# Kernel tuning notes

Hardware: AMD Instinct MI355X
Metric: run time of the kernel (lower is better)

Reference implementation:

```python
import jax, jax.numpy as jnp
import numpy as np

N_NODES = 80000
N_EDGES = 1280000
IN_C, HID_C, OUT_C = 128, 64, 40


def setup_inputs() -> dict:
    key = jax.random.key(0)
    k1, k2, k3, k4 = jax.random.split(key, 4)
    x = jax.random.normal(k1, (N_NODES, IN_C), dtype=jnp.float32)
    edge_index = jax.random.randint(k2, (2, N_EDGES), 0, N_NODES, dtype=jnp.int32)
    W1 = jax.random.normal(k3, (IN_C, HID_C), dtype=jnp.float32) * (1.0 / np.sqrt(IN_C))
    W2 = jax.random.normal(k4, (HID_C, OUT_C), dtype=jnp.float32) * (1.0 / np.sqrt(HID_C))
    return {"x": x, "edge_index": edge_index, "W1": W1, "W2": W2}


def _spmm_add(edge_index, h):
    # adj_t.matmul(h): out[dst] += h[src]  (aggr='add', message = x_j)
    src, dst = edge_index[0], edge_index[1]
    return jax.ops.segment_sum(h[src], dst, num_segments=N_NODES)


def reference(x, edge_index, W1, W2):
    # GCNConv 1: linear (no bias) then add-aggregate SpMM
    h = _spmm_add(edge_index, x @ W1)          # [N, HID]
    h = jax.nn.relu(h)
    # GCNConv 2
    h = _spmm_add(edge_index, h @ W2)          # [N, OUT]
    return jax.nn.log_softmax(h, axis=-1)
```

## Files before the change

kernel.cpp:

```cpp
#include <hip/hip_runtime.h>
#include <hip/hip_bf16.h>
#include <math.h>

#define N_NODES 80000
#define N_EDGES 1280000
#define IN_C 128
#define HID_C 64
#define OUT_C 40

#define KB 157
#define BK_CAP 10240
#define EPT 16

__device__ __forceinline__ float bf_lo(unsigned u) {
    union { unsigned i; float f; } c; c.i = u << 16; return c.f;
}
__device__ __forceinline__ float bf_hi(unsigned u) {
    union { unsigned i; float f; } c; c.i = u & 0xffff0000u; return c.f;
}
__device__ __forceinline__ unsigned pack_bf2(float a, float b) {
    union { float f; unsigned i; } ca, cb; ca.f = a; cb.f = b;
    unsigned ra = (ca.i + 0x7fffu + ((ca.i >> 16) & 1u)) >> 16;
    unsigned rb = (cb.i + 0x7fffu + ((cb.i >> 16) & 1u)) >> 16;
    return ra | (rb << 16);
}

typedef short v8s __attribute__((ext_vector_type(8)));
typedef float v4f __attribute__((ext_vector_type(4)));
union U16 { uint4 u; v8s s; };

__global__ void prep_w_kernel(const float* __restrict__ W1, const float* __restrict__ W2,
                              unsigned* __restrict__ w1t, unsigned* __restrict__ w2t,
                              int* __restrict__ bcnt) {
    const int tid = threadIdx.x;
    if (tid < KB) bcnt[tid] = 0;
    for (int i = tid; i < 4096; i += 256) {
        const int wcol = i >> 6, kk = i & 63;
        w1t[i] = pack_bf2(W1[(2 * kk) * HID_C + wcol], W1[(2 * kk + 1) * HID_C + wcol]);
    }
    for (int i = tid; i < 1536; i += 256) {
        const int wcol = i >> 5, kk = i & 31;
        w2t[i] = (wcol < OUT_C)
            ? pack_bf2(W2[(2 * kk) * OUT_C + wcol], W2[(2 * kk + 1) * OUT_C + wcol])
            : 0u;
    }
}

__global__ void binA_kernel(const int* __restrict__ src, const int* __restrict__ dst,
                            int* __restrict__ bcnt, int* __restrict__ gbuf) {
    __shared__ int lcnt[KB];
    __shared__ int lexcl[KB];
    __shared__ int lbase[KB];
    __shared__ int lcur[KB];
    __shared__ int stage[256 * EPT];
    __shared__ int gaddr[256 * EPT];
    const int tid = threadIdx.x;

    for (int i = tid; i < KB; i += 256) lcnt[i] = 0;
    __syncthreads();

    const int e0 = blockIdx.x * 256 * EPT;
    int my_s[EPT], my_b[EPT], my_dl[EPT];
#pragma unroll
    for (int j = 0; j < EPT; ++j) {
        const int e = e0 + j * 256 + tid;
        if (e < N_EDGES) {
            const int d = dst[e];
            my_s[j] = src[e];
            my_b[j] = d >> 9;
            my_dl[j] = d & 511;
            atomicAdd(&lcnt[my_b[j]], 1);
        } else my_b[j] = -1;
    }
    __syncthreads();

    if (tid < KB) lexcl[tid] = lcnt[tid];
    __syncthreads();
    for (int o = 1; o < KB; o <<= 1) {
        int t = (tid < KB && tid >= o) ? lexcl[tid - o] : 0;
        __syncthreads();
        if (tid < KB) lexcl[tid] += t;
        __syncthreads();
    }
    const int total = lexcl[KB - 1];
    if (tid < KB) {
        lexcl[tid] -= lcnt[tid];
        lbase[tid] = (lcnt[tid] > 0) ? atomicAdd(&bcnt[tid], lcnt[tid]) : 0;
        lcur[tid] = 0;
    }
    __syncthreads();

#pragma unroll
    for (int j = 0; j < EPT; ++j) {
        if (my_b[j] >= 0) {
            const int b = my_b[j];
            const int r = atomicAdd(&lcur[b], 1);
            const int li = lexcl[b] + r;
            stage[li] = (my_s[j] << 9) | my_dl[j];
            int gp = lbase[b] + r;
            if (gp >= BK_CAP) gp = BK_CAP - 1;
            gaddr[li] = b * BK_CAP + gp;
        }
    }
    __syncthreads();

    for (int i = tid; i < total; i += 256)
        gbuf[gaddr[i]] = stage[i];
}

__global__ void binB_kernel(const int* __restrict__ bcnt,
                            const int* __restrict__ gbuf,
                            int* __restrict__ rp, int* __restrict__ col) {
    __shared__ int sc[KB];
    __shared__ int hist[512];
    __shared__ int excl[512];
    __shared__ int cur[512];
    __shared__ int ps[256];
    __shared__ int outb[BK_CAP];
    const int b = blockIdx.x;
    const int tid = threadIdx.x;

    if (tid < KB) sc[tid] = min(bcnt[tid], BK_CAP);
    __syncthreads();
    for (int o = 1; o < KB; o <<= 1) {
        int t = (tid < KB && tid >= o) ? sc[tid - o] : 0;
        __syncthreads();
        if (tid < KB) sc[tid] += t;
        __syncthreads();
    }
    const int n = min(bcnt[b], BK_CAP);
    const int cbase = sc[b] - n;
    const int* __restrict__ my = gbuf + (size_t)b * BK_CAP;

    for (int i = tid; i < 512; i += 256) hist[i] = 0;
    __syncthreads();
    for (int i = tid; i < n; i += 256)
        atomicAdd(&hist[my[i] & 511], 1);
    __syncthreads();

    const int h0 = hist[2 * tid], h1 = hist[2 * tid + 1];
    const int p = h0 + h1;
    ps[tid] = p;
    __syncthreads();
    for (int o = 1; o < 256; o <<= 1) {
        int t = (tid >= o) ? ps[tid - o] : 0;
        __syncthreads();
        ps[tid] += t;
        __syncthreads();
    }
    const int pb = ps[tid] - p;
    excl[2 * tid] = pb;
    excl[2 * tid + 1] = pb + h0;
    cur[2 * tid] = pb;
    cur[2 * tid + 1] = pb + h0;
    __syncthreads();

    for (int i = tid; i < 512; i += 256) {
        const int node = b * 512 + i;
        if (node <= N_NODES) rp[node] = cbase + excl[i];
    }

    for (int i = tid; i < n; i += 256) {
        const int pk = my[i];
        const int pos = atomicAdd(&cur[pk & 511], 1);
        outb[pos] = pk >> 9;
    }
    __syncthreads();
    for (int i = tid; i < n; i += 256)
        col[cbase + i] = outb[i];
}

__global__ __launch_bounds__(256) void gemm1_kernel(const float* __restrict__ x,
                                                    const unsigned* __restrict__ w1t,
                                                    unsigned* __restrict__ h1b) {
    const int wave = threadIdx.x >> 6, lane = threadIdx.x & 63;
    const int nl = lane & 15, quad = lane >> 4;
    const int node = (blockIdx.x * 4 + wave) * 16 + nl;

    v4f acc[4];
#pragma unroll
    for (int q = 0; q < 4; ++q) acc[q] = (v4f){0.f, 0.f, 0.f, 0.f};

#pragma unroll
    for (int kit = 0; kit < 4; ++kit) {
        const float* xp = x + (size_t)node * IN_C + kit * 32 + quad * 8;
        const float4 lo = *(const float4*)xp;
        const float4 hi = *(const float4*)(xp + 4);
        U16 bu;
        bu.u.x = pack_bf2(lo.x, lo.y); bu.u.y = pack_bf2(lo.z, lo.w);
        bu.u.z = pack_bf2(hi.x, hi.y); bu.u.w = pack_bf2(hi.z, hi.w);
#pragma unroll
        for (int mt = 0; mt < 4; ++mt) {
            U16 au;
            au.u = *(const uint4*)(w1t + ((mt * 16 + nl) * 64 + kit * 16 + quad * 4));
            acc[mt] = __builtin_amdgcn_mfma_f32_16x16x32_bf16(au.s, bu.s, acc[mt], 0, 0, 0);
        }
    }
#pragma unroll
    for (int mt = 0; mt < 4; ++mt) {
        uint2 o;
        o.x = pack_bf2(acc[mt][0], acc[mt][1]);
        o.y = pack_bf2(acc[mt][2], acc[mt][3]);
        *(uint2*)(h1b + (size_t)node * 32 + mt * 8 + quad * 2) = o;
    }
}

__global__ void gather64_kernel(const int* __restrict__ rp, const int* __restrict__ col,
                                const unsigned* __restrict__ h1b,
                                unsigned* __restrict__ agg1b) {
    const int lane = threadIdx.x & 63;
    const int wave = threadIdx.x >> 6;
    const int sl = lane & 31;
    const int es = sl >> 3;
    const int cl = sl & 7;
    const int gbase = lane & 32;
    const int node = blockIdx.x * 8 + wave * 2 + (lane >> 5);
    const int b = rp[node], e = rp[node + 1];

    float acc[8];
#pragma unroll
    for (int k = 0; k < 8; ++k) acc[k] = 0.f;

    for (int pos = b; __any(pos < e); pos += 32) {
        const int rem = e - pos;
        const int n = rem > 32 ? 32 : (rem > 0 ? rem : 0);
        const int myIdx = (sl < n) ? col[pos + sl] : 0;
        const int steps = (n + 3) >> 2;
        int j = 0;
        for (; j + 1 < steps; j += 2) {
            const int e0 = (j << 2) + es, e1 = e0 + 4;
            const int s0 = __shfl(myIdx, gbase + e0, 64);
            const int s1 = __shfl(myIdx, gbase + e1, 64);
            uint4 v0, v1;
            const bool g0 = e0 < n, g1 = e1 < n;
            if (g0) v0 = *(const uint4*)(h1b + (size_t)s0 * 32 + cl * 4);
            if (g1) v1 = *(const uint4*)(h1b + (size_t)s1 * 32 + cl * 4);
            if (g0) {
                acc[0] += bf_lo(v0.x); acc[1] += bf_hi(v0.x);
                acc[2] += bf_lo(v0.y); acc[3] += bf_hi(v0.y);
                acc[4] += bf_lo(v0.z); acc[5] += bf_hi(v0.z);
                acc[6] += bf_lo(v0.w); acc[7] += bf_hi(v0.w);
            }
            if (g1) {
                acc[0] += bf_lo(v1.x); acc[1] += bf_hi(v1.x);
                acc[2] += bf_lo(v1.y); acc[3] += bf_hi(v1.y);
                acc[4] += bf_lo(v1.z); acc[5] += bf_hi(v1.z);
                acc[6] += bf_lo(v1.w); acc[7] += bf_hi(v1.w);
            }
        }
        if (j < steps) {
            const int e0 = (j << 2) + es;
            const int s0 = __shfl(myIdx, gbase + e0, 64);
            if (e0 < n) {
                const uint4 v = *(const uint4*)(h1b + (size_t)s0 * 32 + cl * 4);
                acc[0] += bf_lo(v.x); acc[1] += bf_hi(v.x);
                acc[2] += bf_lo(v.y); acc[3] += bf_hi(v.y);
                acc[4] += bf_lo(v.z); acc[5] += bf_hi(v.z);
                acc[6] += bf_lo(v.w); acc[7] += bf_hi(v.w);
            }
        }
    }
#pragma unroll
    for (int k = 0; k < 8; ++k) acc[k] += __shfl_down(acc[k], 16, 64);
#pragma unroll
    for (int k = 0; k < 8; ++k) acc[k] += __shfl_down(acc[k], 8, 64);

    if (sl < 8) {
        uint4 o;
        o.x = pack_bf2(fmaxf(acc[0], 0.f), fmaxf(acc[1], 0.f));
        o.y = pack_bf2(fmaxf(acc[2], 0.f), fmaxf(acc[3], 0.f));
        o.z = pack_bf2(fmaxf(acc[4], 0.f), fmaxf(acc[5], 0.f));
        o.w = pack_bf2(fmaxf(acc[6], 0.f), fmaxf(acc[7], 0.f));
        *(uint4*)(agg1b + (size_t)node * 32 + cl * 4) = o;
    }
}

__global__ __launch_bounds__(256) void gemm2_kernel(const unsigned* __restrict__ agg1b,
                                                    const unsigned* __restrict__ w2t,
                                                    unsigned* __restrict__ h2b) {
    const int wave = threadIdx.x >> 6, lane = threadIdx.x & 63;
    const int nl = lane & 15, quad = lane >> 4;
    const int node = (blockIdx.x * 4 + wave) * 16 + nl;

    v4f acc[3];
#pragma unroll
    for (int q = 0; q < 3; ++q) acc[q] = (v4f){0.f, 0.f, 0.f, 0.f};

#pragma unroll
    for (int kit = 0; kit < 2; ++kit) {
        U16 bu;
        bu.u = *(const uint4*)(agg1b + (size_t)node * 32 + kit * 16 + quad * 4);
#pragma unroll
        for (int mt = 0; mt < 3; ++mt) {
            U16 au;
            au.u = *(const uint4*)(w2t + ((mt * 16 + nl) * 32 + kit * 16 + quad * 4));
            acc[mt] = __builtin_amdgcn_mfma_f32_16x16x32_bf16(au.s, bu.s, acc[mt], 0, 0, 0);
        }
    }
#pragma unroll
    for (int mt = 0; mt < 2; ++mt) {
        uint2 o;
        o.x = pack_bf2(acc[mt][0], acc[mt][1]);
        o.y = pack_bf2(acc[mt][2], acc[mt][3]);
        *(uint2*)(h2b + (size_t)node * 20 + mt * 8 + quad * 2) = o;
    }
    if (quad < 2) {
        uint2 o;
        o.x = pack_bf2(acc[2][0], acc[2][1]);
        o.y = pack_bf2(acc[2][2], acc[2][3]);
        *(uint2*)(h2b + (size_t)node * 20 + 16 + quad * 2) = o;
    }
}

__global__ void gather40_ls_kernel(const int* __restrict__ rp, const int* __restrict__ col,
                                   const unsigned* __restrict__ h2b,
                                   float* __restrict__ out) {
    const int lane = threadIdx.x & 63;
    const int wave = threadIdx.x >> 6;
    const int sl = lane & 15;
    const int es = sl / 5;
    const int cl = sl - es * 5;
    const int gbase = lane & 48;
    const int node = blockIdx.x * 16 + wave * 4 + (lane >> 4);
    const int b = rp[node], e = rp[node + 1];

    float a[8];
#pragma unroll
    for (int k = 0; k < 8; ++k) a[k] = 0.f;

    for (int pos = b; __any(pos < e); pos += 16) {
        const int rem = e - pos;
        const int n = rem > 16 ? 16 : (rem > 0 ? rem : 0);
        const int myIdx = (sl < n) ? col[pos + sl] : 0;
        const int steps = (n + 2) / 3;
        int j = 0;
        for (; j + 1 < steps; j += 2) {
            const int e0 = j * 3 + es, e1 = e0 + 3;
            const int s0 = __shfl(myIdx, gbase + e0, 64);
            const int s1 = __shfl(myIdx, gbase + e1, 64);
            uint4 v0, v1;
            const bool g0 = (es < 3) && (e0 < n), g1 = (es < 3) && (e1 < n);
            if (g0) v0 = *(const uint4*)(h2b + (size_t)s0 * 20 + cl * 4);
            if (g1) v1 = *(const uint4*)(h2b + (size_t)s1 * 20 + cl * 4);
            if (g0) {
                a[0] += bf_lo(v0.x); a[1] += bf_hi(v0.x);
                a[2] += bf_lo(v0.y); a[3] += bf_hi(v0.y);
                a[4] += bf_lo(v0.z); a[5] += bf_hi(v0.z);
                a[6] += bf_lo(v0.w); a[7] += bf_hi(v0.w);
            }
            if (g1) {
                a[0] += bf_lo(v1.x); a[1] += bf_hi(v1.x);
                a[2] += bf_lo(v1.y); a[3] += bf_hi(v1.y);
                a[4] += bf_lo(v1.z); a[5] += bf_hi(v1.z);
                a[6] += bf_lo(v1.w); a[7] += bf_hi(v1.w);
            }
        }
        if (j < steps) {
            const int e0 = j * 3 + es;
            const int s0 = __shfl(myIdx, gbase + e0, 64);
            if ((es < 3) && (e0 < n)) {
                const uint4 v = *(const uint4*)(h2b + (size_t)s0 * 20 + cl * 4);
                a[0] += bf_lo(v.x); a[1] += bf_hi(v.x);
                a[2] += bf_lo(v.y); a[3] += bf_hi(v.y);
                a[4] += bf_lo(v.z); a[5] += bf_hi(v.z);
                a[6] += bf_lo(v.w); a[7] += bf_hi(v.w);
            }
        }
    }
#pragma unroll
    for (int k = 0; k < 8; ++k) {
        const float u = __shfl_down(a[k], 5, 64);
        const float w = __shfl_down(a[k], 10, 64);
        a[k] += u + w;
    }

    const bool own = sl < 5;
    float m = -INFINITY;
    if (own) {
        m = a[0];
#pragma unroll
        for (int k = 1; k < 8; ++k) m = fmaxf(m, a[k]);
    }
    const float m0 = __shfl(m, gbase + 0, 64), m1 = __shfl(m, gbase + 1, 64);
    const float m2 = __shfl(m, gbase + 2, 64), m3 = __shfl(m, gbase + 3, 64);
    const float m4 = __shfl(m, gbase + 4, 64);
    const float gm = fmaxf(fmaxf(fmaxf(m0, m1), fmaxf(m2, m3)), m4);

    float s = 0.f;
    if (own) {
#pragma unroll
        for (int k = 0; k < 8; ++k) s += __expf(a[k] - gm);
    }
    const float s0 = __shfl(s, gbase + 0, 64), s1 = __shfl(s, gbase + 1, 64);
    const float s2 = __shfl(s, gbase + 2, 64), s3 = __shfl(s, gbase + 3, 64);
    const float s4 = __shfl(s, gbase + 4, 64);
    const float ls = __logf(s0 + s1 + s2 + s3 + s4) + gm;

    if (own) {
        float* op = out + (size_t)node * OUT_C + cl * 8;
        *(float4*)op = make_float4(a[0] - ls, a[1] - ls, a[2] - ls, a[3] - ls);
        *(float4*)(op + 4) = make_float4(a[4] - ls, a[5] - ls, a[6] - ls, a[7] - ls);
    }
}

extern "C" void kernel_launch(void* const* d_in, const int* in_sizes, int n_in,
                              void* d_out, int out_size, void* d_ws, size_t ws_size,
                              hipStream_t stream) {
    const float* x  = (const float*)d_in[0];
    const int* eidx = (const int*)d_in[1];
    const float* W1 = (const float*)d_in[2];
    const float* W2 = (const float*)d_in[3];
    float* out = (float*)d_out;

    const int* src = eidx;
    const int* dst = eidx + N_EDGES;

    unsigned* h1b   = (unsigned*)d_ws;
    unsigned* agg1b = h1b + (size_t)N_NODES * 32;
    unsigned* h2b   = agg1b + (size_t)N_NODES * 32;
    int*      gbuf  = (int*)(h2b + (size_t)N_NODES * 20);
    int*      col   = gbuf + (size_t)KB * BK_CAP;
    int*      rp    = col + N_EDGES;
    int*      bcnt  = rp + (N_NODES + 1);
    unsigned* w1t   = (unsigned*)(bcnt + KB);
    unsigned* w2t   = w1t + 4096;

    prep_w_kernel<<<1, 256, 0, stream>>>(W1, W2, w1t, w2t, bcnt);
    binA_kernel<<<(N_EDGES + 256 * EPT - 1) / (256 * EPT), 256, 0, stream>>>(src, dst, bcnt, gbuf);
    binB_kernel<<<KB, 256, 0, stream>>>(bcnt, gbuf, rp, col);

    gemm1_kernel<<<N_NODES / 64, 256, 0, stream>>>(x, w1t, h1b);
    gather64_kernel<<<N_NODES / 8, 256, 0, stream>>>(rp, col, h1b, agg1b);
    gemm2_kernel<<<N_NODES / 64, 256, 0, stream>>>(agg1b, w2t, h2b);
    gather40_ls_kernel<<<N_NODES / 16, 256, 0, stream>>>(rp, col, h2b, out);
}
```

Baseline: 196.0 us.

## Fuse first-layer gather with second GEMM via shared memory; fully unroll gather loops

Merges the 64-channel neighbor gather and the second MFMA GEMM into a single 512-thread kernel. Each block aggregates 16 nodes into LDS, then one wave runs the W2 MFMA on them, so the agg1b intermediate is no longer written to and read back from global memory and one launch is dropped. The gather inner loops in both gather kernels are also rewritten as fixed-count fully unrolled loops with per-iteration guards. In exchange, only one wave of eight does the GEMM stage while the rest sit idle after the barrier, and the unrolled loops may run predicated-off iterations for low-degree nodes.

```diff
diff --git a/kernel.cpp b/kernel.cpp
--- a/kernel.cpp
+++ b/kernel.cpp
@@ -205,16 +205,20 @@
     }
 }
 
-__global__ void gather64_kernel(const int* __restrict__ rp, const int* __restrict__ col,
-                                const unsigned* __restrict__ h1b,
-                                unsigned* __restrict__ agg1b) {
-    const int lane = threadIdx.x & 63;
-    const int wave = threadIdx.x >> 6;
+__global__ __launch_bounds__(512) void gather64_gemm2_kernel(
+        const int* __restrict__ rp, const int* __restrict__ col,
+        const unsigned* __restrict__ h1b, const unsigned* __restrict__ w2t,
+        unsigned* __restrict__ h2b) {
+    __shared__ float aggs[16][66];
+    const int tid = threadIdx.x;
+    const int lane = tid & 63;
+    const int wave = tid >> 6;
     const int sl = lane & 31;
     const int es = sl >> 3;
     const int cl = sl & 7;
     const int gbase = lane & 32;
-    const int node = blockIdx.x * 8 + wave * 2 + (lane >> 5);
+    const int nloc = wave * 2 + (lane >> 5);
+    const int node = blockIdx.x * 16 + nloc;
     const int b = rp[node], e = rp[node + 1];
 
     float acc[8];
@@ -225,34 +229,12 @@
         const int rem = e - pos;
         const int n = rem > 32 ? 32 : (rem > 0 ? rem : 0);
         const int myIdx = (sl < n) ? col[pos + sl] : 0;
-        const int steps = (n + 3) >> 2;
-        int j = 0;
-        for (; j + 1 < steps; j += 2) {
-            const int e0 = (j << 2) + es, e1 = e0 + 4;
-            const int s0 = __shfl(myIdx, gbase + e0, 64);
-            const int s1 = __shfl(myIdx, gbase + e1, 64);
-            uint4 v0, v1;
-            const bool g0 = e0 < n, g1 = e1 < n;
-            if (g0) v0 = *(const uint4*)(h1b + (size_t)s0 * 32 + cl * 4);
-            if (g1) v1 = *(const uint4*)(h1b + (size_t)s1 * 32 + cl * 4);
-            if (g0) {
-                acc[0] += bf_lo(v0.x); acc[1] += bf_hi(v0.x);
-                acc[2] += bf_lo(v0.y); acc[3] += bf_hi(v0.y);
-                acc[4] += bf_lo(v0.z); acc[5] += bf_hi(v0.z);
-                acc[6] += bf_lo(v0.w); acc[7] += bf_hi(v0.w);
-            }
-            if (g1) {
-                acc[0] += bf_lo(v1.x); acc[1] += bf_hi(v1.x);
-                acc[2] += bf_lo(v1.y); acc[3] += bf_hi(v1.y);
-                acc[4] += bf_lo(v1.z); acc[5] += bf_hi(v1.z);
-                acc[6] += bf_lo(v1.w); acc[7] += bf_hi(v1.w);
-            }
-        }
-        if (j < steps) {
-            const int e0 = (j << 2) + es;
-            const int s0 = __shfl(myIdx, gbase + e0, 64);
-            if (e0 < n) {
-                const uint4 v = *(const uint4*)(h1b + (size_t)s0 * 32 + cl * 4);
+#pragma unroll
+        for (int j = 0; j < 8; ++j) {
+            const int ei = (j << 2) + es;
+            const int s = __shfl(myIdx, gbase + ei, 64);
+            if (ei < n) {
+                const uint4 v = *(const uint4*)(h1b + (size_t)s * 32 + cl * 4);
                 acc[0] += bf_lo(v.x); acc[1] += bf_hi(v.x);
                 acc[2] += bf_lo(v.y); acc[3] += bf_hi(v.y);
                 acc[4] += bf_lo(v.z); acc[5] += bf_hi(v.z);
@@ -266,49 +248,48 @@
     for (int k = 0; k < 8; ++k) acc[k] += __shfl_down(acc[k], 8, 64);
 
     if (sl < 8) {
-        uint4 o;
-        o.x = pack_bf2(fmaxf(acc[0], 0.f), fmaxf(acc[1], 0.f));
-        o.y = pack_bf2(fmaxf(acc[2], 0.f), fmaxf(acc[3], 0.f));
-        o.z = pack_bf2(fmaxf(acc[4], 0.f), fmaxf(acc[5], 0.f));
-        o.w = pack_bf2(fmaxf(acc[6], 0.f), fmaxf(acc[7], 0.f));
-        *(uint4*)(agg1b + (size_t)node * 32 + cl * 4) = o;
-    }
-}
-
-__global__ __launch_bounds__(256) void gemm2_kernel(const unsigned* __restrict__ agg1b,
-                                                    const unsigned* __restrict__ w2t,
-                                                    unsigned* __restrict__ h2b) {
-    const int wave = threadIdx.x >> 6, lane = threadIdx.x & 63;
-    const int nl = lane & 15, quad = lane >> 4;
-    const int node = (blockIdx.x * 4 + wave) * 16 + nl;
-
-    v4f acc[3];
-#pragma unroll
-    for (int q = 0; q < 3; ++q) acc[q] = (v4f){0.f, 0.f, 0.f, 0.f};
-
-#pragma unroll
-    for (int kit = 0; kit < 2; ++kit) {
-        U16 bu;
-        bu.u = *(const uint4*)(agg1b + (size_t)node * 32 + kit * 16 + quad * 4);
-#pragma unroll
-        for (int mt = 0; mt < 3; ++mt) {
-            U16 au;
-            au.u = *(const uint4*)(w2t + ((mt * 16 + nl) * 32 + kit * 16 + quad * 4));
-            acc[mt] = __builtin_amdgcn_mfma_f32_16x16x32_bf16(au.s, bu.s, acc[mt], 0, 0, 0);
-        }
-    }
-#pragma unroll
-    for (int mt = 0; mt < 2; ++mt) {
-        uint2 o;
-        o.x = pack_bf2(acc[mt][0], acc[mt][1]);
-        o.y = pack_bf2(acc[mt][2], acc[mt][3]);
-        *(uint2*)(h2b + (size_t)node * 20 + mt * 8 + quad * 2) = o;
-    }
-    if (quad < 2) {
-        uint2 o;
-        o.x = pack_bf2(acc[2][0], acc[2][1]);
-        o.y = pack_bf2(acc[2][2], acc[2][3]);
-        *(uint2*)(h2b + (size_t)node * 20 + 16 + quad * 2) = o;
+        float* p = &aggs[nloc][cl * 8];
+        p[0] = fmaxf(acc[0], 0.f); p[1] = fmaxf(acc[1], 0.f);
+        p[2] = fmaxf(acc[2], 0.f); p[3] = fmaxf(acc[3], 0.f);
+        p[4] = fmaxf(acc[4], 0.f); p[5] = fmaxf(acc[5], 0.f);
+        p[6] = fmaxf(acc[6], 0.f); p[7] = fmaxf(acc[7], 0.f);
+    }
+    __syncthreads();
+
+    if (tid < 64) {
+        const int nl = lane & 15, quad = lane >> 4;
+        const int onode = blockIdx.x * 16 + nl;
+
+        v4f c[3];
+#pragma unroll
+        for (int q = 0; q < 3; ++q) c[q] = (v4f){0.f, 0.f, 0.f, 0.f};
+
+#pragma unroll
+        for (int kit = 0; kit < 2; ++kit) {
+            const float* p = &aggs[nl][kit * 32 + quad * 8];
+            U16 bu;
+            bu.u.x = pack_bf2(p[0], p[1]); bu.u.y = pack_bf2(p[2], p[3]);
+            bu.u.z = pack_bf2(p[4], p[5]); bu.u.w = pack_bf2(p[6], p[7]);
+#pragma unroll
+            for (int mt = 0; mt < 3; ++mt) {
+                U16 au;
+                au.u = *(const uint4*)(w2t + ((mt * 16 + nl) * 32 + kit * 16 + quad * 4));
+                c[mt] = __builtin_amdgcn_mfma_f32_16x16x32_bf16(au.s, bu.s, c[mt], 0, 0, 0);
+            }
+        }
+#pragma unroll
+        for (int mt = 0; mt < 2; ++mt) {
+            uint2 o;
+            o.x = pack_bf2(c[mt][0], c[mt][1]);
+            o.y = pack_bf2(c[mt][2], c[mt][3]);
+            *(uint2*)(h2b + (size_t)onode * 20 + mt * 8 + quad * 2) = o;
+        }
+        if (quad < 2) {
+            uint2 o;
+            o.x = pack_bf2(c[2][0], c[2][1]);
+            o.y = pack_bf2(c[2][2], c[2][3]);
+            *(uint2*)(h2b + (size_t)onode * 20 + 16 + quad * 2) = o;
+        }
     }
 }
 
@@ -332,34 +313,12 @@
         const int rem = e - pos;
         const int n = rem > 16 ? 16 : (rem > 0 ? rem : 0);
         const int myIdx = (sl < n) ? col[pos + sl] : 0;
-        const int steps = (n + 2) / 3;
-        int j = 0;
-        for (; j + 1 < steps; j += 2) {
-            const int e0 = j * 3 + es, e1 = e0 + 3;
-            const int s0 = __shfl(myIdx, gbase + e0, 64);
-            const int s1 = __shfl(myIdx, gbase + e1, 64);
-            uint4 v0, v1;
-            const bool g0 = (es < 3) && (e0 < n), g1 = (es < 3) && (e1 < n);
-            if (g0) v0 = *(const uint4*)(h2b + (size_t)s0 * 20 + cl * 4);
-            if (g1) v1 = *(const uint4*)(h2b + (size_t)s1 * 20 + cl * 4);
-            if (g0) {
-                a[0] += bf_lo(v0.x); a[1] += bf_hi(v0.x);
-                a[2] += bf_lo(v0.y); a[3] += bf_hi(v0.y);
-                a[4] += bf_lo(v0.z); a[5] += bf_hi(v0.z);
-                a[6] += bf_lo(v0.w); a[7] += bf_hi(v0.w);
-            }
-            if (g1) {
-                a[0] += bf_lo(v1.x); a[1] += bf_hi(v1.x);
-                a[2] += bf_lo(v1.y); a[3] += bf_hi(v1.y);
-                a[4] += bf_lo(v1.z); a[5] += bf_hi(v1.z);
-                a[6] += bf_lo(v1.w); a[7] += bf_hi(v1.w);
-            }
-        }
-        if (j < steps) {
-            const int e0 = j * 3 + es;
-            const int s0 = __shfl(myIdx, gbase + e0, 64);
-            if ((es < 3) && (e0 < n)) {
-                const uint4 v = *(const uint4*)(h2b + (size_t)s0 * 20 + cl * 4);
+#pragma unroll
+        for (int j = 0; j < 6; ++j) {
+            const int ei = j * 3 + es;
+            const int s = __shfl(myIdx, gbase + ei, 64);
+            if ((es < 3) && (ei < n)) {
+                const uint4 v = *(const uint4*)(h2b + (size_t)s * 20 + cl * 4);
                 a[0] += bf_lo(v.x); a[1] += bf_hi(v.x);
                 a[2] += bf_lo(v.y); a[3] += bf_hi(v.y);
                 a[4] += bf_lo(v.z); a[5] += bf_hi(v.z);
@@ -416,8 +375,7 @@
     const int* dst = eidx + N_EDGES;
 
     unsigned* h1b   = (unsigned*)d_ws;
-    unsigned* agg1b = h1b + (size_t)N_NODES * 32;
-    unsigned* h2b   = agg1b + (size_t)N_NODES * 32;
+    unsigned* h2b   = h1b + (size_t)N_NODES * 32;
     int*      gbuf  = (int*)(h2b + (size_t)N_NODES * 20);
     int*      col   = gbuf + (size_t)KB * BK_CAP;
     int*      rp    = col + N_EDGES;
@@ -430,7 +388,6 @@
     binB_kernel<<<KB, 256, 0, stream>>>(bcnt, gbuf, rp, col);
 
     gemm1_kernel<<<N_NODES / 64, 256, 0, stream>>>(x, w1t, h1b);
-    gather64_kernel<<<N_NODES / 8, 256, 0, stream>>>(rp, col, h1b, agg1b);
-    gemm2_kernel<<<N_NODES / 64, 256, 0, stream>>>(agg1b, w2t, h2b);
+    gather64_gemm2_kernel<<<N_NODES / 16, 512, 0, stream>>>(rp, col, h1b, w2t, h2b);
     gather40_ls_kernel<<<N_NODES / 16, 256, 0, stream>>>(rp, col, h2b, out);
 }
```

Measured after the change: 197.9 us. No clear change (+1.0%).
